# Kernel optimization log

Hardware: AMD Instinct MI355X
Metric: run time of the kernel (lower is better)

## Reference

```python
import jax, jax.numpy as jnp
import numpy as np


def setup_inputs() -> dict:
    key = jax.random.key(0)
    k1, k2 = jax.random.split(key)
    DIM = 33
    lut_count = jnp.zeros((3, DIM, DIM, DIM), dtype=jnp.int32)
    lut = jax.random.normal(k1, (3, DIM, DIM, DIM), dtype=jnp.float32)
    x = jax.random.uniform(k2, (8, 3, 1024, 1024), dtype=jnp.float32)
    return {"lut_count": lut_count, "lut": lut, "x": x}


def _trilinear_lut(lut, x):
    # lut: [3, dim, dim, dim] stored so that flat index = r + g*dim + b*dim^2
    # x:   [B, 3, H, W] with values in [0, 1)
    dim = lut.shape[-1]
    shift = dim * dim * dim
    binsize = 1.000001 / (dim - 1)

    r, g, b = x[:, 0], x[:, 1], x[:, 2]              # each [B, H, W]
    r_id = jnp.floor(r / binsize).astype(jnp.int32)
    g_id = jnp.floor(g / binsize).astype(jnp.int32)
    b_id = jnp.floor(b / binsize).astype(jnp.int32)

    # fractional offsets within the cell (== fmod(v, binsize)/binsize)
    rd = r / binsize - r_id
    gd = g / binsize - g_id
    bd = b / binsize - b_id

    id000 = r_id + g_id * dim + b_id * dim * dim      # [B, H, W]
    flat_lut = lut.reshape(3, shift)                  # [3, dim^3]

    w000 = (1 - rd) * (1 - gd) * (1 - bd)
    w100 = rd * (1 - gd) * (1 - bd)
    w010 = (1 - rd) * gd * (1 - bd)
    w110 = rd * gd * (1 - bd)
    w001 = (1 - rd) * (1 - gd) * bd
    w101 = rd * (1 - gd) * bd
    w011 = (1 - rd) * gd * bd
    w111 = rd * gd * bd

    def corner(offset, w):
        # gather all 3 output channels at once: [3, B, H, W] -> [B, 3, H, W]
        vals = jnp.moveaxis(flat_lut[:, id000 + offset], 0, 1)
        return w[:, None] * vals

    d2 = dim * dim
    out = (corner(0, w000) + corner(1, w100) +
           corner(dim, w010) + corner(dim + 1, w110) +
           corner(d2, w001) + corner(d2 + 1, w101) +
           corner(d2 + dim, w011) + corner(d2 + dim + 1, w111))
    return out


def reference(lut_count, lut, x):
    # Original forward returns (lut, output); lut_count is only used for
    # usage counting in count_map and does not affect the forward math.
    output = _trilinear_lut(lut, x)
    return (lut, output)
```

## Files before the change

### kernel.cpp

```cpp
#include <hip/hip_runtime.h>


typedef float f32x4 __attribute__((ext_vector_type(4)));

#define DIM    33
#define D2     (DIM * DIM)
#define SHIFT  (DIM * DIM * DIM)
#define LUT_ELEMS (3 * SHIFT)
#define NCELL  32768
#define RECF   24
#define PLANE  1048576
#define NPIX   (8 * PLANE)

__global__ __launch_bounds__(256) void build_cells_kernel(
    const float* __restrict__ lut, float* __restrict__ cells) {
    int t = blockIdx.x * 256 + threadIdx.x;
    if (t >= NCELL * RECF) return;
    int cell   = t / RECF;
    int j      = t - cell * RECF;
    int corner = j / 3;
    int ch     = j - corner * 3;
    int ri = cell & 31, gi = (cell >> 5) & 31, bi = cell >> 10;
    int dr = corner & 1, dg = (corner >> 1) & 1, db = corner >> 2;
    cells[t] = lut[ch * SHIFT + (bi + db) * D2 + (gi + dg) * DIM + (ri + dr)];
}

__device__ __forceinline__ void lut_one(const float* __restrict__ cells,
                                        float r, float g, float b,
                                        float& outr, float& outg, float& outb) {
    const float BIN = (float)(1.000001 / 32.0);
    float rs = r / BIN, gs = g / BIN, bs = b / BIN;
    float rf = floorf(rs), gf = floorf(gs), bf = floorf(bs);
    float rd = rs - rf, gd = gs - gf, bd = bs - bf;
    int ri = (int)rf, gi = (int)gf, bi = (int)bf;
    int cell = (bi << 10) | (gi << 5) | ri;

    const f32x4* rec = (const f32x4*)(cells + cell * 24);
    f32x4 q0 = rec[0], q1 = rec[1], q2 = rec[2];
    f32x4 q3 = rec[3], q4 = rec[4], q5 = rec[5];
    float v[24];
    *(f32x4*)(v +  0) = q0;
    *(f32x4*)(v +  4) = q1;
    *(f32x4*)(v +  8) = q2;
    *(f32x4*)(v + 12) = q3;
    *(f32x4*)(v + 16) = q4;
    *(f32x4*)(v + 20) = q5;

    float omr = 1.0f - rd, omg = 1.0f - gd, omb = 1.0f - bd;
    float w000 = omr * omg * omb;
    float w100 = rd  * omg * omb;
    float w010 = omr * gd  * omb;
    float w110 = rd  * gd  * omb;
    float w001 = omr * omg * bd;
    float w101 = rd  * omg * bd;
    float w011 = omr * gd  * bd;
    float w111 = rd  * gd  * bd;

    outr = w000*v[0] + w100*v[3] + w010*v[6]  + w110*v[9]  + w001*v[12] + w101*v[15] + w011*v[18] + w111*v[21];
    outg = w000*v[1] + w100*v[4] + w010*v[7]  + w110*v[10] + w001*v[13] + w101*v[16] + w011*v[19] + w111*v[22];
    outb = w000*v[2] + w100*v[5] + w010*v[8]  + w110*v[11] + w001*v[14] + w101*v[17] + w011*v[20] + w111*v[23];
}

__global__ __launch_bounds__(256) void apply_A_kernel(
    const float* __restrict__ x, const float* __restrict__ cells,
    float* __restrict__ out) {
    int t = blockIdx.x * 256 + threadIdx.x;
    int b = t >> 20;
    int p = t & (PLANE - 1);
    const float* xb = x + (size_t)b * (3 * PLANE) + p;
    float r  = __builtin_nontemporal_load(xb);
    float g  = __builtin_nontemporal_load(xb + PLANE);
    float bl = __builtin_nontemporal_load(xb + 2 * PLANE);
    float orr, og, obl;
    lut_one(cells, r, g, bl, orr, og, obl);
    float* ob = out + (size_t)b * (3 * PLANE) + p;
    __builtin_nontemporal_store(orr, ob);
    __builtin_nontemporal_store(og,  ob + PLANE);
    __builtin_nontemporal_store(obl, ob + 2 * PLANE);
}

__global__ __launch_bounds__(256) void apply_B_kernel(
    const float* __restrict__ x, const float* __restrict__ cells,
    float* __restrict__ out) {
    int t = blockIdx.x * 256 + threadIdx.x;
    int b = t >> 18;
    int p = (t & ((PLANE / 4) - 1)) << 2;
    const float* xb = x + (size_t)b * (3 * PLANE) + p;
    f32x4 r4 = __builtin_nontemporal_load((const f32x4*)(xb));
    f32x4 g4 = __builtin_nontemporal_load((const f32x4*)(xb + PLANE));
    f32x4 b4 = __builtin_nontemporal_load((const f32x4*)(xb + 2 * PLANE));

    f32x4 o0, o1, o2;
    #pragma unroll
    for (int i = 0; i < 4; ++i) {
        float orr, og, ob;
        lut_one(cells, r4[i], g4[i], b4[i], orr, og, ob);
        o0[i] = orr; o1[i] = og; o2[i] = ob;
    }

    float* o = out + (size_t)b * (3 * PLANE) + p;
    __builtin_nontemporal_store(o0, (f32x4*)(o));
    __builtin_nontemporal_store(o1, (f32x4*)(o + PLANE));
    __builtin_nontemporal_store(o2, (f32x4*)(o + 2 * PLANE));
}

__global__ __launch_bounds__(256) void apply_direct_kernel(
    const float* __restrict__ x, const float* __restrict__ lut,
    float* __restrict__ out) {
    int t = blockIdx.x * 256 + threadIdx.x;
    int b = t >> 20;
    int p = t & (PLANE - 1);
    const float* xb = x + (size_t)b * (3 * PLANE) + p;
    float r  = xb[0];
    float g  = xb[PLANE];
    float bl = xb[2 * PLANE];

    const float BIN = (float)(1.000001 / 32.0);
    float rs = r / BIN, gs = g / BIN, bs = bl / BIN;
    float rf = floorf(rs), gf = floorf(gs), bf = floorf(bs);
    float rd = rs - rf, gd = gs - gf, bd = bs - bf;
    int ri = (int)rf, gi = (int)gf, bi = (int)bf;
    int id000 = ri + gi * DIM + bi * D2;

    float omr = 1.0f - rd, omg = 1.0f - gd, omb = 1.0f - bd;
    float w000 = omr*omg*omb, w100 = rd*omg*omb, w010 = omr*gd*omb, w110 = rd*gd*omb;
    float w001 = omr*omg*bd,  w101 = rd*omg*bd,  w011 = omr*gd*bd,  w111 = rd*gd*bd;

    float* ob = out + (size_t)b * (3 * PLANE) + p;
    #pragma unroll
    for (int ch = 0; ch < 3; ++ch) {
        const float* L = lut + ch * SHIFT + id000;
        float acc = w000 * L[0]        + w100 * L[1]
                  + w010 * L[DIM]      + w110 * L[DIM + 1]
                  + w001 * L[D2]       + w101 * L[D2 + 1]
                  + w011 * L[D2 + DIM] + w111 * L[D2 + DIM + 1];
        ob[(size_t)ch * PLANE] = acc;
    }
}

extern "C" void kernel_launch(void* const* d_in, const int* in_sizes, int n_in,
                              void* d_out, int out_size, void* d_ws, size_t ws_size,
                              hipStream_t stream) {
    const float* lut = (const float*)d_in[1];
    const float* x   = (const float*)d_in[2];
    float* out = (float*)d_out;

    (void)hipMemcpyAsync(out, lut, (size_t)LUT_ELEMS * sizeof(float),
                         hipMemcpyDeviceToDevice, stream);

    float* outimg = out + LUT_ELEMS;
    const size_t cells_bytes = (size_t)NCELL * RECF * sizeof(float);

    if (ws_size >= cells_bytes) {
        float* cells = (float*)d_ws;
        build_cells_kernel<<<(NCELL * RECF + 255) / 256, 256, 0, stream>>>(lut, cells);

        const int half_pix = NPIX / 2;
        apply_A_kernel<<<half_pix / 256, 256, 0, stream>>>(x, cells, outimg);

        const size_t off = (size_t)4 * (3 * PLANE);
        apply_B_kernel<<<(half_pix / 4) / 256, 256, 0, stream>>>(
            x + off, cells, outimg + off);
    } else {
        apply_direct_kernel<<<NPIX / 256, 256, 0, stream>>>(x, lut, outimg);
    }
}
```

Measured before the change: 277.3 us.

## Gather LUT cell records cooperatively into swizzled shared memory with 128-byte padding

Pads each precomputed cell record from 96 to 128 bytes. A new apply kernel has groups of four lanes fetch one pixel's record as coalesced 16-byte chunks into an XOR-swizzled LDS buffer, so each thread then reads its own record without bank conflicts. The aim is to replace the scattered per-thread 96-byte gathers with more efficient wave-cooperative global loads. In exchange it adds two block barriers and 32 KB of LDS per block, which may lower occupancy, and it drops the split A/B vectorised apply path.

```diff
diff --git a/kernel.cpp b/kernel.cpp
--- a/kernel.cpp
+++ b/kernel.cpp
@@ -8,43 +8,72 @@
 #define SHIFT  (DIM * DIM * DIM)
 #define LUT_ELEMS (3 * SHIFT)
 #define NCELL  32768
-#define RECF   24
 #define PLANE  1048576
 #define NPIX   (8 * PLANE)
 
-__global__ __launch_bounds__(256) void build_cells_kernel(
+__global__ __launch_bounds__(256) void build_cells128_kernel(
     const float* __restrict__ lut, float* __restrict__ cells) {
     int t = blockIdx.x * 256 + threadIdx.x;
-    if (t >= NCELL * RECF) return;
-    int cell   = t / RECF;
-    int j      = t - cell * RECF;
-    int corner = j / 3;
-    int ch     = j - corner * 3;
-    int ri = cell & 31, gi = (cell >> 5) & 31, bi = cell >> 10;
-    int dr = corner & 1, dg = (corner >> 1) & 1, db = corner >> 2;
-    cells[t] = lut[ch * SHIFT + (bi + db) * D2 + (gi + dg) * DIM + (ri + dr)];
-}
-
-__device__ __forceinline__ void lut_one(const float* __restrict__ cells,
-                                        float r, float g, float b,
-                                        float& outr, float& outg, float& outb) {
+    int cell = t >> 5;
+    int j = t & 31;
+    float v = 0.0f;
+    if (j < 24) {
+        int corner = j / 3;
+        int ch = j - corner * 3;
+        int ri = cell & 31, gi = (cell >> 5) & 31, bi = cell >> 10;
+        int dr = corner & 1, dg = (corner >> 1) & 1, db = corner >> 2;
+        v = lut[ch * SHIFT + (bi + db) * D2 + (gi + dg) * DIM + (ri + dr)];
+    }
+    cells[t] = v;
+}
+
+__global__ __launch_bounds__(256) void apply_coop_kernel(
+    const float* __restrict__ x, const float* __restrict__ cells,
+    float* __restrict__ out) {
+    __shared__ float recs[256 * 32];
+    __shared__ int cellIdx[256];
+
+    const int tid = threadIdx.x;
+    const int t = blockIdx.x * 256 + tid;
+    const int b = t >> 20;
+    const int p = t & (PLANE - 1);
+    const float* xb = x + (size_t)b * (3 * PLANE) + p;
+    float r  = __builtin_nontemporal_load(xb);
+    float g  = __builtin_nontemporal_load(xb + PLANE);
+    float bl = __builtin_nontemporal_load(xb + 2 * PLANE);
+
     const float BIN = (float)(1.000001 / 32.0);
-    float rs = r / BIN, gs = g / BIN, bs = b / BIN;
+    float rs = r / BIN, gs = g / BIN, bs = bl / BIN;
     float rf = floorf(rs), gf = floorf(gs), bf = floorf(bs);
     float rd = rs - rf, gd = gs - gf, bd = bs - bf;
-    int ri = (int)rf, gi = (int)gf, bi = (int)bf;
-    int cell = (bi << 10) | (gi << 5) | ri;
-
-    const f32x4* rec = (const f32x4*)(cells + cell * 24);
-    f32x4 q0 = rec[0], q1 = rec[1], q2 = rec[2];
-    f32x4 q3 = rec[3], q4 = rec[4], q5 = rec[5];
+    int cell = (((int)bf) << 10) | (((int)gf) << 5) | ((int)rf);
+    cellIdx[tid] = cell;
+    __syncthreads();
+
+    const int lane = tid & 63;
+    const int wavebase = tid & 192;
+    #pragma unroll
+    for (int r4 = 0; r4 < 4; ++r4) {
+        int pl = wavebase + r4 * 16 + (lane >> 2);
+        int c  = cellIdx[pl];
+        int k  = pl & 7;
+        const f32x4* src = (const f32x4*)(cells + (size_t)c * 32);
+        int cl0 = lane & 3;
+        int cl1 = 4 + (lane & 3);
+        f32x4 v0 = src[cl0];
+        f32x4 v1 = src[cl1];
+        f32x4* row = (f32x4*)(recs + pl * 32);
+        row[cl0 ^ k] = v0;
+        row[cl1 ^ k] = v1;
+    }
+    __syncthreads();
+
+    int k = tid & 7;
+    const f32x4* row = (const f32x4*)(recs + tid * 32);
     float v[24];
-    *(f32x4*)(v +  0) = q0;
-    *(f32x4*)(v +  4) = q1;
-    *(f32x4*)(v +  8) = q2;
-    *(f32x4*)(v + 12) = q3;
-    *(f32x4*)(v + 16) = q4;
-    *(f32x4*)(v + 20) = q5;
+    #pragma unroll
+    for (int c = 0; c < 6; ++c)
+        *(f32x4*)(v + 4 * c) = row[c ^ k];
 
     float omr = 1.0f - rd, omg = 1.0f - gd, omb = 1.0f - bd;
     float w000 = omr * omg * omb;
@@ -56,9 +85,27 @@
     float w011 = omr * gd  * bd;
     float w111 = rd  * gd  * bd;
 
-    outr = w000*v[0] + w100*v[3] + w010*v[6]  + w110*v[9]  + w001*v[12] + w101*v[15] + w011*v[18] + w111*v[21];
-    outg = w000*v[1] + w100*v[4] + w010*v[7]  + w110*v[10] + w001*v[13] + w101*v[16] + w011*v[19] + w111*v[22];
-    outb = w000*v[2] + w100*v[5] + w010*v[8]  + w110*v[11] + w001*v[14] + w101*v[17] + w011*v[20] + w111*v[23];
+    float orr = w000*v[0] + w100*v[3] + w010*v[6]  + w110*v[9]  + w001*v[12] + w101*v[15] + w011*v[18] + w111*v[21];
+    float og  = w000*v[1] + w100*v[4] + w010*v[7]  + w110*v[10] + w001*v[13] + w101*v[16] + w011*v[19] + w111*v[22];
+    float obl = w000*v[2] + w100*v[5] + w010*v[8]  + w110*v[11] + w001*v[14] + w101*v[17] + w011*v[20] + w111*v[23];
+
+    float* ob = out + (size_t)b * (3 * PLANE) + p;
+    __builtin_nontemporal_store(orr, ob);
+    __builtin_nontemporal_store(og,  ob + PLANE);
+    __builtin_nontemporal_store(obl, ob + 2 * PLANE);
+}
+
+__global__ __launch_bounds__(256) void build_cells96_kernel(
+    const float* __restrict__ lut, float* __restrict__ cells) {
+    int t = blockIdx.x * 256 + threadIdx.x;
+    if (t >= NCELL * 24) return;
+    int cell = t / 24;
+    int j = t - cell * 24;
+    int corner = j / 3;
+    int ch = j - corner * 3;
+    int ri = cell & 31, gi = (cell >> 5) & 31, bi = cell >> 10;
+    int dr = corner & 1, dg = (corner >> 1) & 1, db = corner >> 2;
+    cells[t] = lut[ch * SHIFT + (bi + db) * D2 + (gi + dg) * DIM + (ri + dr)];
 }
 
 __global__ __launch_bounds__(256) void apply_A_kernel(
@@ -71,37 +118,34 @@
     float r  = __builtin_nontemporal_load(xb);
     float g  = __builtin_nontemporal_load(xb + PLANE);
     float bl = __builtin_nontemporal_load(xb + 2 * PLANE);
-    float orr, og, obl;
-    lut_one(cells, r, g, bl, orr, og, obl);
+
+    const float BIN = (float)(1.000001 / 32.0);
+    float rs = r / BIN, gs = g / BIN, bs = bl / BIN;
+    float rf = floorf(rs), gf = floorf(gs), bf = floorf(bs);
+    float rd = rs - rf, gd = gs - gf, bd = bs - bf;
+    int cell = (((int)bf) << 10) | (((int)gf) << 5) | ((int)rf);
+
+    const f32x4* rec = (const f32x4*)(cells + cell * 24);
+    float v[24];
+    *(f32x4*)(v +  0) = rec[0];
+    *(f32x4*)(v +  4) = rec[1];
+    *(f32x4*)(v +  8) = rec[2];
+    *(f32x4*)(v + 12) = rec[3];
+    *(f32x4*)(v + 16) = rec[4];
+    *(f32x4*)(v + 20) = rec[5];
+
+    float omr = 1.0f - rd, omg = 1.0f - gd, omb = 1.0f - bd;
+    float w000 = omr*omg*omb, w100 = rd*omg*omb, w010 = omr*gd*omb, w110 = rd*gd*omb;
+    float w001 = omr*omg*bd,  w101 = rd*omg*bd,  w011 = omr*gd*bd,  w111 = rd*gd*bd;
+
+    float orr = w000*v[0] + w100*v[3] + w010*v[6]  + w110*v[9]  + w001*v[12] + w101*v[15] + w011*v[18] + w111*v[21];
+    float og  = w000*v[1] + w100*v[4] + w010*v[7]  + w110*v[10] + w001*v[13] + w101*v[16] + w011*v[19] + w111*v[22];
+    float obl = w000*v[2] + w100*v[5] + w010*v[8]  + w110*v[11] + w001*v[14] + w101*v[17] + w011*v[20] + w111*v[23];
+
     float* ob = out + (size_t)b * (3 * PLANE) + p;
     __builtin_nontemporal_store(orr, ob);
     __builtin_nontemporal_store(og,  ob + PLANE);
     __builtin_nontemporal_store(obl, ob + 2 * PLANE);
-}
-
-__global__ __launch_bounds__(256) void apply_B_kernel(
-    const float* __restrict__ x, const float* __restrict__ cells,
-    float* __restrict__ out) {
-    int t = blockIdx.x * 256 + threadIdx.x;
-    int b = t >> 18;
-    int p = (t & ((PLANE / 4) - 1)) << 2;
-    const float* xb = x + (size_t)b * (3 * PLANE) + p;
-    f32x4 r4 = __builtin_nontemporal_load((const f32x4*)(xb));
-    f32x4 g4 = __builtin_nontemporal_load((const f32x4*)(xb + PLANE));
-    f32x4 b4 = __builtin_nontemporal_load((const f32x4*)(xb + 2 * PLANE));
-
-    f32x4 o0, o1, o2;
-    #pragma unroll
-    for (int i = 0; i < 4; ++i) {
-        float orr, og, ob;
-        lut_one(cells, r4[i], g4[i], b4[i], orr, og, ob);
-        o0[i] = orr; o1[i] = og; o2[i] = ob;
-    }
-
-    float* o = out + (size_t)b * (3 * PLANE) + p;
-    __builtin_nontemporal_store(o0, (f32x4*)(o));
-    __builtin_nontemporal_store(o1, (f32x4*)(o + PLANE));
-    __builtin_nontemporal_store(o2, (f32x4*)(o + 2 * PLANE));
 }
 
 __global__ __launch_bounds__(256) void apply_direct_kernel(
@@ -119,8 +163,7 @@
     float rs = r / BIN, gs = g / BIN, bs = bl / BIN;
     float rf = floorf(rs), gf = floorf(gs), bf = floorf(bs);
     float rd = rs - rf, gd = gs - gf, bd = bs - bf;
-    int ri = (int)rf, gi = (int)gf, bi = (int)bf;
-    int id000 = ri + gi * DIM + bi * D2;
+    int id000 = (int)rf + (int)gf * DIM + (int)bf * D2;
 
     float omr = 1.0f - rd, omg = 1.0f - gd, omb = 1.0f - bd;
     float w000 = omr*omg*omb, w100 = rd*omg*omb, w010 = omr*gd*omb, w110 = rd*gd*omb;
@@ -149,18 +192,17 @@
                          hipMemcpyDeviceToDevice, stream);
 
     float* outimg = out + LUT_ELEMS;
-    const size_t cells_bytes = (size_t)NCELL * RECF * sizeof(float);
-
-    if (ws_size >= cells_bytes) {
+    const size_t bytes128 = (size_t)NCELL * 32 * sizeof(float);
+    const size_t bytes96  = (size_t)NCELL * 24 * sizeof(float);
+
+    if (ws_size >= bytes128) {
         float* cells = (float*)d_ws;
-        build_cells_kernel<<<(NCELL * RECF + 255) / 256, 256, 0, stream>>>(lut, cells);
-
-        const int half_pix = NPIX / 2;
-        apply_A_kernel<<<half_pix / 256, 256, 0, stream>>>(x, cells, outimg);
-
-        const size_t off = (size_t)4 * (3 * PLANE);
-        apply_B_kernel<<<(half_pix / 4) / 256, 256, 0, stream>>>(
-            x + off, cells, outimg + off);
+        build_cells128_kernel<<<NCELL * 32 / 256, 256, 0, stream>>>(lut, cells);
+        apply_coop_kernel<<<NPIX / 256, 256, 0, stream>>>(x, cells, outimg);
+    } else if (ws_size >= bytes96) {
+        float* cells = (float*)d_ws;
+        build_cells96_kernel<<<(NCELL * 24 + 255) / 256, 256, 0, stream>>>(lut, cells);
+        apply_A_kernel<<<NPIX / 256, 256, 0, stream>>>(x, cells, outimg);
     } else {
         apply_direct_kernel<<<NPIX / 256, 256, 0, stream>>>(x, lut, outimg);
     }
```

New measurement: 246.1 us. -11.3%, faster.
